# Optimization experiments

Hardware: AMD Instinct MI355X
Metric: run time of the kernel (lower is better)

## Reference

```python
import jax, jax.numpy as jnp
import numpy as np

DIM_Q = 1024
DIM_KV = 768
N_HEADS = 4


def setup_inputs() -> dict:
    key = jax.random.key(0)
    ks = jax.random.split(key, 7)
    b, lq, lkv = 4, 2048, 2048
    q = jax.random.normal(ks[0], (b, lq, DIM_Q), dtype=jnp.float32)
    kv = jax.random.normal(ks[1], (b, lkv, DIM_KV), dtype=jnp.float32)
    s_q = 1.0 / np.sqrt(DIM_Q)
    s_kv = 1.0 / np.sqrt(DIM_KV)
    Wq = jax.random.normal(ks[2], (DIM_Q, DIM_Q), dtype=jnp.float32) * s_q
    Wk = jax.random.normal(ks[3], (DIM_Q, DIM_KV), dtype=jnp.float32) * s_kv
    Wv = jax.random.normal(ks[4], (DIM_Q, DIM_KV), dtype=jnp.float32) * s_kv
    Wo = jax.random.normal(ks[5], (DIM_Q, DIM_Q), dtype=jnp.float32) * s_q
    bo = jax.random.normal(ks[6], (DIM_Q,), dtype=jnp.float32) * 0.01
    return {"q": q, "kv": kv, "Wq": Wq, "Wk": Wk, "Wv": Wv, "Wo": Wo, "bo": bo}


def _split_heads(x):
    # [b, l, d] -> [b, h, l, d/h]
    b, l, d = x.shape
    return x.reshape(b, l, N_HEADS, d // N_HEADS).transpose(0, 2, 1, 3)


def reference(q, kv, Wq, Wk, Wv, Wo, bo):
    qp = q @ Wq.T               # [b, lq, dim_q]
    kp = kv @ Wk.T              # [b, lkv, dim_q]
    vp = kv @ Wv.T              # [b, lkv, dim_q]
    qh, kh, vh = _split_heads(qp), _split_heads(kp), _split_heads(vp)
    scale = (DIM_Q // N_HEADS) ** (-0.5)
    scores = jnp.einsum('bhqd,bhkd->bhqk', qh, kh) * scale
    attn = jax.nn.softmax(scores, axis=-1)
    ctx = jnp.einsum('bhqk,bhkd->bhqd', attn, vh)  # [b, h, lq, hd]
    b, h, lq, hd = ctx.shape
    ctx = ctx.transpose(0, 2, 1, 3).reshape(b, lq, h * hd)
    return ctx @ Wo.T + bo
```

## Files before the change

kernel.cpp:

```cpp
#include <hip/hip_runtime.h>

#define DIMQ 1024
#define NH 4
#define HD 256
#define BSZ 4
#define LQ 2048
#define LKV 2048
#define KVN 2048

typedef __attribute__((ext_vector_type(8))) short bf16x8;
typedef __attribute__((ext_vector_type(4))) float f32x4;

__device__ inline unsigned short f32_to_bf16(float f) {
  union { float f; unsigned u; } v; v.f = f;
  unsigned u = v.u;
  return (unsigned short)((u + 0x7fffu + ((u >> 16) & 1u)) >> 16);
}

__device__ inline uint4 ld8cvt(const float* p, float scale) {
  const float4 a = *(const float4*)p;
  const float4 b = *(const float4*)(p + 4);
  union { unsigned short s[8]; uint4 v; } r;
  r.s[0] = f32_to_bf16(a.x * scale); r.s[1] = f32_to_bf16(a.y * scale);
  r.s[2] = f32_to_bf16(a.z * scale); r.s[3] = f32_to_bf16(a.w * scale);
  r.s[4] = f32_to_bf16(b.x * scale); r.s[5] = f32_to_bf16(b.y * scale);
  r.s[6] = f32_to_bf16(b.z * scale); r.s[7] = f32_to_bf16(b.w * scale);
  return r.v;
}

__device__ __forceinline__ void gl2lds16(const void* gptr, void* lptr) {
  __builtin_amdgcn_global_load_lds(
      (const __attribute__((address_space(1))) void*)gptr,
      (__attribute__((address_space(3))) void*)lptr, 16, 0, 0);
}

__global__ __launch_bounds__(256)
void cvt5(const float* s0, const float* s1, const float* s2, const float* s3,
          const float* s4, unsigned short* d0, unsigned short* d1,
          unsigned short* d2, unsigned short* d3, unsigned short* d4,
          long n0, long n1, long n2, long n3, long n4,
          float c0, float c1, float c2, float c3, float c4) {
  const float* s; unsigned short* d; long n; float c;
  switch (blockIdx.y) {
    case 0: s = s0; d = d0; n = n0; c = c0; break;
    case 1: s = s1; d = d1; n = n1; c = c1; break;
    case 2: s = s2; d = d2; n = n2; c = c2; break;
    case 3: s = s3; d = d3; n = n3; c = c3; break;
    default: s = s4; d = d4; n = n4; c = c4; break;
  }
  long i = ((long)blockIdx.x * 256 + threadIdx.x) * 8;
  if (i < n) *(uint4*)(d + i) = ld8cvt(s + i, c);
}

__global__ __launch_bounds__(256)
void transpose_k(const unsigned short* __restrict__ vp,
                 unsigned short* __restrict__ vpT,
                 int src_stride, int src_off) {
  __shared__ unsigned short T[64][72];
  const int l0g = blockIdx.x * 64;
  const int b = l0g / LKV, l0 = l0g % LKV;
  const int n0 = blockIdx.y * 64;
  const int tid = threadIdx.x;
  const int r = tid >> 3, c = tid & 7;
#pragma unroll
  for (int p = 0; p < 2; ++p) {
    int row = p * 32 + r;
    *(uint4*)&T[row][c * 8] =
        *(const uint4*)(vp + (size_t)(l0g + row) * src_stride + src_off + n0 + c * 8);
  }
  __syncthreads();
#pragma unroll
  for (int p = 0; p < 2; ++p) {
    int n = p * 32 + r;
    union { unsigned short s[8]; uint4 v; } t;
#pragma unroll
    for (int j = 0; j < 8; ++j) t.s[j] = T[c * 8 + j][n];
    *(uint4*)(vpT + ((size_t)b * DIMQ + n0 + n) * LKV + l0 + c * 8) = t.v;
  }
}

template<typename TOUT, bool HAS_BIAS>
__global__ __launch_bounds__(256)
void gemm_bt(const unsigned short* __restrict__ A,
             const unsigned short* __restrict__ Bm,
             const float* __restrict__ bias,
             TOUT* __restrict__ C,
             int M, int N, int K) {
  __shared__ alignas(16) unsigned short As[128 * 64];
  __shared__ alignas(16) unsigned short Bs[128 * 64];
  const int tid = threadIdx.x;
  const int lane = tid & 63;
  const int wave = tid >> 6;
  const int wr = (wave >> 1) * 64, wc = (wave & 1) * 64;
  const int l15 = lane & 15, quad = lane >> 4;
  const int srow = lane >> 3, scol = lane & 7;
  const int m0 = blockIdx.x * 128;
  const int n0 = blockIdx.y * 128;

  f32x4 acc[4][4] = {};
  for (int k0 = 0; k0 < K; k0 += 64) {
    __syncthreads();
#pragma unroll
    for (int i = 0; i < 4; ++i) {
      int c = wave * 4 + i;
      gl2lds16(A + (size_t)(m0 + c * 8 + srow) * K + k0 + scol * 8, As + c * 512);
      gl2lds16(Bm + (size_t)(n0 + c * 8 + srow) * K + k0 + scol * 8, Bs + c * 512);
    }
    __syncthreads();
#pragma unroll
    for (int kh = 0; kh < 2; ++kh) {
      bf16x8 af[4], bfr[4];
#pragma unroll
      for (int i = 0; i < 4; ++i)
        af[i] = *(const bf16x8*)(As + (wr + i * 16 + l15) * 64 + kh * 32 + quad * 8);
#pragma unroll
      for (int j = 0; j < 4; ++j)
        bfr[j] = *(const bf16x8*)(Bs + (wc + j * 16 + l15) * 64 + kh * 32 + quad * 8);
#pragma unroll
      for (int i = 0; i < 4; ++i)
#pragma unroll
        for (int j = 0; j < 4; ++j)
          acc[i][j] = __builtin_amdgcn_mfma_f32_16x16x32_bf16(af[i], bfr[j], acc[i][j], 0, 0, 0);
    }
  }

#pragma unroll
  for (int j = 0; j < 4; ++j) {
    int n = n0 + wc + j * 16 + l15;
    float bv = 0.f;
    if (HAS_BIAS) bv = bias[n];
#pragma unroll
    for (int i = 0; i < 4; ++i) {
      int mb = m0 + wr + i * 16 + quad * 4;
#pragma unroll
      for (int r = 0; r < 4; ++r) {
        float v = acc[i][j][r] + bv;
        if constexpr (sizeof(TOUT) == 2)
          C[(size_t)(mb + r) * N + n] = f32_to_bf16(v);
        else
          C[(size_t)(mb + r) * N + n] = v;
      }
    }
  }
}

__global__ __launch_bounds__(256, 2)
void attn(const unsigned short* __restrict__ qp,
          const unsigned short* __restrict__ kpv,
          const unsigned short* __restrict__ vpT,
          unsigned short* __restrict__ ctx) {
  __shared__ alignas(16) unsigned short Ks[8 * 64 * 32];
  __shared__ alignas(16) unsigned short Vt[2 * 256 * 32];
  __shared__ alignas(16) unsigned short Ps[4][16 * 72];
  const int tid = threadIdx.x, lane = tid & 63, wave = tid >> 6;
  const int l15 = lane & 15, quad = lane >> 4;
  const int lr = lane >> 2, lc = lane & 3;
  const int b = blockIdx.z, h = blockIdx.y;
  const int q0 = blockIdx.x * 64;
  const size_t base = (size_t)b * LQ * DIMQ + h * HD;

  bf16x8 qf[8];
  const unsigned short* qrow = qp + base + (size_t)(q0 + wave * 16 + l15) * DIMQ;
#pragma unroll
  for (int s = 0; s < 8; ++s)
    qf[s] = *(const bf16x8*)(qrow + s * 32 + quad * 8);

  f32x4 oacc[16] = {};
  float lrow[4] = {0.f, 0.f, 0.f, 0.f};

  const unsigned short* kb = kpv + (size_t)b * LKV * KVN + h * HD;
  const unsigned short* vtb = vpT + ((size_t)b * DIMQ + h * HD) * LKV;

  for (int kv0 = 0; kv0 < LKV; kv0 += 64) {
    __syncthreads();
#pragma unroll
    for (int i = 0; i < 8; ++i) {
      int c = i * 4 + wave, s = c & 7, g = c >> 3;
      gl2lds16(kb + (size_t)(kv0 + g * 16 + lr) * KVN + s * 32 + lc * 8,
               Ks + s * 2048 + g * 512);
    }
#pragma unroll
    for (int i = 0; i < 8; ++i) {
      int c = i * 4 + wave, u = c >> 4, g = c & 15;
      gl2lds16(vtb + (size_t)(g * 16 + lr) * LKV + kv0 + u * 32 + lc * 8,
               Vt + u * 8192 + g * 512);
    }
    __syncthreads();

    f32x4 sacc[4] = {};
#pragma unroll
    for (int s = 0; s < 8; ++s)
#pragma unroll
      for (int j = 0; j < 4; ++j) {
        bf16x8 kf = *(const bf16x8*)(Ks + s * 2048 + (j * 16 + l15) * 32 + quad * 8);
        sacc[j] = __builtin_amdgcn_mfma_f32_16x16x32_bf16(qf[s], kf, sacc[j], 0, 0, 0);
      }

#pragma unroll
    for (int i = 0; i < 4; ++i) {
      float ps = 0.f;
#pragma unroll
      for (int j = 0; j < 4; ++j) {
        float p = __expf(sacc[j][i]);
        ps += p;
        Ps[wave][(quad * 4 + i) * 72 + j * 16 + l15] = f32_to_bf16(p);
      }
      lrow[i] += ps;
    }

#pragma unroll
    for (int u = 0; u < 2; ++u) {
      bf16x8 pf = *(const bf16x8*)(Ps[wave] + l15 * 72 + u * 32 + quad * 8);
#pragma unroll
      for (int t = 0; t < 16; ++t) {
        bf16x8 vf = *(const bf16x8*)(Vt + u * 8192 + (t * 16 + l15) * 32 + quad * 8);
        oacc[t] = __builtin_amdgcn_mfma_f32_16x16x32_bf16(pf, vf, oacc[t], 0, 0, 0);
      }
    }
  }

  float inv[4];
#pragma unroll
  for (int r = 0; r < 4; ++r) {
    float l = lrow[r];
    l += __shfl_xor(l, 1);
    l += __shfl_xor(l, 2);
    l += __shfl_xor(l, 4);
    l += __shfl_xor(l, 8);
    inv[r] = 1.0f / l;
  }
  unsigned short* cb = ctx + base;
#pragma unroll
  for (int t = 0; t < 16; ++t) {
    int col = t * 16 + l15;
#pragma unroll
    for (int r = 0; r < 4; ++r) {
      int row = q0 + wave * 16 + quad * 4 + r;
      cb[(size_t)row * DIMQ + col] = f32_to_bf16(oacc[t][r] * inv[r]);
    }
  }
}

extern "C" void kernel_launch(void* const* d_in, const int* in_sizes, int n_in,
                              void* d_out, int out_size, void* d_ws, size_t ws_size,
                              hipStream_t stream) {
  const float* q  = (const float*)d_in[0];
  const float* kv = (const float*)d_in[1];
  const float* Wq = (const float*)d_in[2];
  const float* Wk = (const float*)d_in[3];
  const float* Wv = (const float*)d_in[4];
  const float* Wo = (const float*)d_in[5];
  const float* bo = (const float*)d_in[6];
  float* out = (float*)d_out;

  const long NQ = (long)BSZ * LQ * DIMQ;
  const long NKV = (long)BSZ * LKV * 768;
  const long NWQ = (long)DIMQ * DIMQ;
  const long NWK = (long)DIMQ * 768;

  unsigned short* q_bf = (unsigned short*)d_out;
  unsigned short* kpv  = (unsigned short*)d_out;
  unsigned short* kv_bf = (unsigned short*)d_ws;
  unsigned short* ctx   = kv_bf;
  unsigned short* Wq_bf = kv_bf + NQ;
  unsigned short* Wk_bf = Wq_bf + NWQ;
  unsigned short* Wv_bf = Wk_bf + NWK;
  unsigned short* Wo_bf = Wv_bf + NWK;
  unsigned short* qp    = Wo_bf + NWQ;
  unsigned short* vpT   = qp + NQ;

  dim3 blk(256);
  const int M = BSZ * LQ;

  cvt5<<<dim3(3072, 5), blk, 0, stream>>>(kv, Wq, Wk, Wv, Wo,
                                          kv_bf, Wq_bf, Wk_bf, Wv_bf, Wo_bf,
                                          NKV, NWQ, NWK, NWK, NWQ,
                                          1.0f, 0.0625f, 1.0f, 1.0f, 1.0f);
  cvt5<<<dim3(4096, 1), blk, 0, stream>>>(q, nullptr, nullptr, nullptr, nullptr,
                                          q_bf, nullptr, nullptr, nullptr, nullptr,
                                          NQ, 0, 0, 0, 0,
                                          1.0f, 0.f, 0.f, 0.f, 0.f);
  gemm_bt<unsigned short, false><<<dim3(M/128, DIMQ/128), blk, 0, stream>>>(q_bf, Wq_bf, nullptr, qp, M, DIMQ, 1024);
  gemm_bt<unsigned short, false><<<dim3(M/128, KVN/128), blk, 0, stream>>>(kv_bf, Wk_bf, nullptr, kpv, M, KVN, 768);
  transpose_k<<<dim3(M/64, DIMQ/64), blk, 0, stream>>>(kpv, vpT, KVN, 1024);
  attn<<<dim3(LQ/64, NH, BSZ), blk, 0, stream>>>(qp, kpv, vpT, ctx);
  gemm_bt<float, true><<<dim3(M/128, DIMQ/128), blk, 0, stream>>>(ctx, Wo_bf, bo, out, M, DIMQ, 1024);
}
```

Measured before the change: 327.3 us.

## Split attention waves into 2x2 grid over query rows and key/head-dim columns

Repartitions the attention block's four waves from one 16-row query strip per wave into a 2x2 layout. Each wave now computes 32 query rows against half of the 64 KV columns for scores, and half of the 256 head-dim columns for the PV product. Each K and V fragment read from LDS now feeds two MFMAs instead of one, cutting LDS read traffic per MFMA. The cost is a shared P tile with an extra block barrier per iteration, a cross-wave row-sum reduction through LDS at the end, and twice the Q fragment registers per wave.

Result: faster. 318.7 us (-2.6%).

```diff
diff --git a/kernel.cpp b/kernel.cpp
--- a/kernel.cpp
+++ b/kernel.cpp
@@ -151,22 +151,29 @@
           unsigned short* __restrict__ ctx) {
   __shared__ alignas(16) unsigned short Ks[8 * 64 * 32];
   __shared__ alignas(16) unsigned short Vt[2 * 256 * 32];
-  __shared__ alignas(16) unsigned short Ps[4][16 * 72];
+  __shared__ alignas(16) unsigned short Ps[64 * 72];
+  __shared__ float Ls[64][2];
   const int tid = threadIdx.x, lane = tid & 63, wave = tid >> 6;
   const int l15 = lane & 15, quad = lane >> 4;
   const int lr = lane >> 2, lc = lane & 3;
+  const int qh = wave >> 1;
+  const int kvh = wave & 1;
   const int b = blockIdx.z, h = blockIdx.y;
   const int q0 = blockIdx.x * 64;
   const size_t base = (size_t)b * LQ * DIMQ + h * HD;
 
-  bf16x8 qf[8];
-  const unsigned short* qrow = qp + base + (size_t)(q0 + wave * 16 + l15) * DIMQ;
-#pragma unroll
-  for (int s = 0; s < 8; ++s)
-    qf[s] = *(const bf16x8*)(qrow + s * 32 + quad * 8);
-
-  f32x4 oacc[16] = {};
-  float lrow[4] = {0.f, 0.f, 0.f, 0.f};
+  bf16x8 qf[2][8];
+#pragma unroll
+  for (int im = 0; im < 2; ++im) {
+    const unsigned short* qrow =
+        qp + base + (size_t)(q0 + qh * 32 + im * 16 + l15) * DIMQ;
+#pragma unroll
+    for (int s = 0; s < 8; ++s)
+      qf[im][s] = *(const bf16x8*)(qrow + s * 32 + quad * 8);
+  }
+
+  f32x4 oacc[2][8] = {};
+  float lrow[2][4] = {};
 
   const unsigned short* kb = kpv + (size_t)b * LKV * KVN + h * HD;
   const unsigned short* vtb = vpT + ((size_t)b * DIMQ + h * HD) * LKV;
@@ -187,58 +194,69 @@
     }
     __syncthreads();
 
-    f32x4 sacc[4] = {};
-#pragma unroll
-    for (int s = 0; s < 8; ++s)
-#pragma unroll
-      for (int j = 0; j < 4; ++j) {
-        bf16x8 kf = *(const bf16x8*)(Ks + s * 2048 + (j * 16 + l15) * 32 + quad * 8);
-        sacc[j] = __builtin_amdgcn_mfma_f32_16x16x32_bf16(qf[s], kf, sacc[j], 0, 0, 0);
+    f32x4 sacc[2][2] = {};
+#pragma unroll
+    for (int s = 0; s < 8; ++s) {
+      bf16x8 kf0 = *(const bf16x8*)(Ks + s * 2048 + (kvh * 32 + l15) * 32 + quad * 8);
+      bf16x8 kf1 = *(const bf16x8*)(Ks + s * 2048 + (kvh * 32 + 16 + l15) * 32 + quad * 8);
+      sacc[0][0] = __builtin_amdgcn_mfma_f32_16x16x32_bf16(qf[0][s], kf0, sacc[0][0], 0, 0, 0);
+      sacc[0][1] = __builtin_amdgcn_mfma_f32_16x16x32_bf16(qf[0][s], kf1, sacc[0][1], 0, 0, 0);
+      sacc[1][0] = __builtin_amdgcn_mfma_f32_16x16x32_bf16(qf[1][s], kf0, sacc[1][0], 0, 0, 0);
+      sacc[1][1] = __builtin_amdgcn_mfma_f32_16x16x32_bf16(qf[1][s], kf1, sacc[1][1], 0, 0, 0);
+    }
+
+#pragma unroll
+    for (int im = 0; im < 2; ++im)
+#pragma unroll
+      for (int i = 0; i < 4; ++i) {
+        int row = qh * 32 + im * 16 + quad * 4 + i;
+        float p0 = __expf(sacc[im][0][i]);
+        float p1 = __expf(sacc[im][1][i]);
+        Ps[row * 72 + kvh * 32 + l15] = f32_to_bf16(p0);
+        Ps[row * 72 + kvh * 32 + 16 + l15] = f32_to_bf16(p1);
+        lrow[im][i] += p0 + p1;
       }
-
+    __syncthreads();
+
+#pragma unroll
+    for (int u = 0; u < 2; ++u) {
+      bf16x8 pf0 = *(const bf16x8*)(Ps + (qh * 32 + l15) * 72 + u * 32 + quad * 8);
+      bf16x8 pf1 = *(const bf16x8*)(Ps + (qh * 32 + 16 + l15) * 72 + u * 32 + quad * 8);
+#pragma unroll
+      for (int jn = 0; jn < 8; ++jn) {
+        bf16x8 vf = *(const bf16x8*)(Vt + u * 8192 + (kvh * 128 + jn * 16 + l15) * 32 + quad * 8);
+        oacc[0][jn] = __builtin_amdgcn_mfma_f32_16x16x32_bf16(pf0, vf, oacc[0][jn], 0, 0, 0);
+        oacc[1][jn] = __builtin_amdgcn_mfma_f32_16x16x32_bf16(pf1, vf, oacc[1][jn], 0, 0, 0);
+      }
+    }
+  }
+
+#pragma unroll
+  for (int im = 0; im < 2; ++im)
 #pragma unroll
     for (int i = 0; i < 4; ++i) {
-      float ps = 0.f;
-#pragma unroll
-      for (int j = 0; j < 4; ++j) {
-        float p = __expf(sacc[j][i]);
-        ps += p;
-        Ps[wave][(quad * 4 + i) * 72 + j * 16 + l15] = f32_to_bf16(p);
+      float l = lrow[im][i];
+      l += __shfl_xor(l, 1);
+      l += __shfl_xor(l, 2);
+      l += __shfl_xor(l, 4);
+      l += __shfl_xor(l, 8);
+      if (l15 == 0) Ls[qh * 32 + im * 16 + quad * 4 + i][kvh] = l;
+    }
+  __syncthreads();
+
+  unsigned short* cb = ctx + base;
+#pragma unroll
+  for (int im = 0; im < 2; ++im)
+#pragma unroll
+    for (int r = 0; r < 4; ++r) {
+      int row = qh * 32 + im * 16 + quad * 4 + r;
+      float inv = 1.0f / (Ls[row][0] + Ls[row][1]);
+#pragma unroll
+      for (int jn = 0; jn < 8; ++jn) {
+        int col = kvh * 128 + jn * 16 + l15;
+        cb[(size_t)(q0 + row) * DIMQ + col] = f32_to_bf16(oacc[im][jn][r] * inv);
       }
-      lrow[i] += ps;
-    }
-
-#pragma unroll
-    for (int u = 0; u < 2; ++u) {
-      bf16x8 pf = *(const bf16x8*)(Ps[wave] + l15 * 72 + u * 32 + quad * 8);
-#pragma unroll
-      for (int t = 0; t < 16; ++t) {
-        bf16x8 vf = *(const bf16x8*)(Vt + u * 8192 + (t * 16 + l15) * 32 + quad * 8);
-        oacc[t] = __builtin_amdgcn_mfma_f32_16x16x32_bf16(pf, vf, oacc[t], 0, 0, 0);
-      }
-    }
-  }
-
-  float inv[4];
-#pragma unroll
-  for (int r = 0; r < 4; ++r) {
-    float l = lrow[r];
-    l += __shfl_xor(l, 1);
-    l += __shfl_xor(l, 2);
-    l += __shfl_xor(l, 4);
-    l += __shfl_xor(l, 8);
-    inv[r] = 1.0f / l;
-  }
-  unsigned short* cb = ctx + base;
-#pragma unroll
-  for (int t = 0; t < 16; ++t) {
-    int col = t * 16 + l15;
-#pragma unroll
-    for (int r = 0; r < 4; ++r) {
-      int row = q0 + wave * 16 + quad * 4 + r;
-      cb[(size_t)row * DIMQ + col] = f32_to_bf16(oacc[t][r] * inv[r]);
-    }
-  }
+    }
 }
 
 extern "C" void kernel_launch(void* const* d_in, const int* in_sizes, int n_in,
```
